# Kernel optimization log

Hardware: AMD Instinct MI355X
Metric: run time of the kernel (lower is better)

Reference implementation:

```python
import jax, jax.numpy as jnp
import numpy as np
from jax import lax

B, L, D = 4, 4096, 1024
EXPAND, K = 2, 4
INNER = D * EXPAND  # 2048


def setup_inputs() -> dict:
    key = jax.random.key(0)
    k0, k1, k2, k3, k4 = jax.random.split(key, 5)
    s = 0.02
    return {
        "x": jax.random.normal(k0, (B, L, D), jnp.float32),
        "W_in": jax.random.normal(k1, (D, 2 * INNER), jnp.float32) * s,
        "conv_w": jax.random.normal(k2, (INNER, 1, K), jnp.float32) * s,  # depthwise [out, in/groups=1, k]
        "conv_b": jax.random.normal(k3, (INNER,), jnp.float32) * s,
        "W_out": jax.random.normal(k4, (INNER, D), jnp.float32) * s,
    }


def reference(x, W_in, conv_w, conv_b, W_out):
    # Linear (no bias): [B,L,D] -> [B,L,2*INNER]
    h = jnp.einsum("bld,df->blf", x, W_in)
    # GLU(dim=-1): first half gated by sigmoid of second half
    a, g = jnp.split(h, 2, axis=-1)
    h = a * jax.nn.sigmoid(g)  # [B,L,INNER]
    # depthwise causal Conv1d: torch pads both sides by K-1 then slices [:, :, :L],
    # which equals left-padding by K-1 only.
    hc = jnp.transpose(h, (0, 2, 1))  # [B,INNER,L]
    y = lax.conv_general_dilated(
        hc, conv_w,
        window_strides=(1,),
        padding=[(K - 1, 0)],
        dimension_numbers=("NCH", "OIH", "NCH"),
        feature_group_count=INNER,
    ) + conv_b[None, :, None]  # [B,INNER,L]
    y = jax.nn.silu(y)
    y = jnp.transpose(y, (0, 2, 1))  # [B,L,INNER]
    # Output linear (no bias): [B,L,INNER] -> [B,L,D]
    return jnp.einsum("blf,fd->bld", y, W_out)
```

## Files before the change

### kernel.cpp

```cpp
#include <hip/hip_runtime.h>
#include <hip/hip_bf16.h>

constexpr int B_ = 4, L_ = 4096, D_ = 1024, INNER_ = 2048;
constexpr int M_ = B_ * L_;
constexpr int N1_ = 2 * INNER_;

typedef __attribute__((ext_vector_type(4))) float f32x4;
typedef __attribute__((ext_vector_type(8))) short short8;

#define DEV static __device__ __forceinline__

DEV short f2bfs(float f) {
  __hip_bfloat16 h = __float2bfloat16(f);
  return __builtin_bit_cast(short, h);
}
DEV float bfs2f(short s) {
  unsigned int u = ((unsigned int)(unsigned short)s) << 16;
  return __builtin_bit_cast(float, u);
}

DEV void gload_lds16(const void* g, void* l) {
  __builtin_amdgcn_global_load_lds(
      (const __attribute__((address_space(1))) unsigned int*)g,
      (__attribute__((address_space(3))) unsigned int*)l,
      16, 0, 0);
}

constexpr int VMW8 = 0x0F78;
constexpr int VMW4 = 0x0F74;
constexpr int VMW0 = 0x0F70;

__global__ void k_cvt(const float4* __restrict__ in, short4* __restrict__ out, int n4) {
  int i = blockIdx.x * blockDim.x + threadIdx.x;
  if (i >= n4) return;
  float4 v = in[i];
  short4 o;
  o.x = f2bfs(v.x); o.y = f2bfs(v.y); o.z = f2bfs(v.z); o.w = f2bfs(v.w);
  out[i] = o;
}

__global__ void k_transpose_cvt(const float* __restrict__ W, short* __restrict__ Wt,
                                int R, int C) {
  __shared__ short tile[32][33];
  int tx = threadIdx.x & 31;
  int ty = threadIdx.x >> 5;
  int c0 = blockIdx.x * 32;
  int r0 = blockIdx.y * 32;
#pragma unroll
  for (int i = 0; i < 32; i += 8)
    tile[ty + i][tx] = f2bfs(W[(size_t)(r0 + ty + i) * C + (c0 + tx)]);
  __syncthreads();
#pragma unroll
  for (int i = 0; i < 32; i += 8)
    Wt[(size_t)(c0 + ty + i) * R + (r0 + tx)] = tile[tx][ty + i];
}

template<int K, bool GLU>
__global__ __launch_bounds__(512, 2) void k_gemm_pipe(
    const short* __restrict__ A, const short* __restrict__ Bt,
    short* __restrict__ OutBf, float* __restrict__ OutF) {
  extern __shared__ char lds[];
  constexpr int NT = K / 32;
  const int tid = threadIdx.x;
  const int wid = tid >> 6, lane = tid & 63;
  const int l16 = lane & 15, kg = lane >> 4;
  const int wr = wid >> 1, wc = wid & 1;

  const int bid = (int)blockIdx.x;
  const int j = bid & 7;
  const int s = bid >> 3;
  const int r = s >> 5;
  const int t = s & 31;
  const int bm = j * 8 + (t >> 2);
  const int bn = r * 4 + (t & 3);
  const int m0 = bm * 256;

  const short* pA[2];
  const short* pB[2];
  int ldsA[2], ldsB[2];
#pragma unroll
  for (int h = 0; h < 2; ++h) {
    int p = h * 512 + wid * 64 + lane;
    int q = p ^ ((p >> 3) & 7);
    int row = q >> 2, c = q & 3;
    pA[h] = A + (size_t)(m0 + row) * K + c * 8;
    int gb;
    if constexpr (GLU) {
      gb = bn * 128 + ((row >> 7) << 6) + (row & 63) + (((row >> 6) & 1) ? 2048 : 0);
    } else {
      gb = bn * 256 + row;
    }
    pB[h] = Bt + (size_t)gb * K + c * 8;
    ldsA[h] = h * 8192 + wid * 1024;
    ldsB[h] = 16384 + h * 8192 + wid * 1024;
  }

  int offA[4], offB[8];
#pragma unroll
  for (int m = 0; m < 4; ++m) {
    int row = wr * 64 + m * 16 + l16;
    int ch = row * 4 + kg;
    offA[m] = (ch ^ ((ch >> 3) & 7)) * 16;
  }
#pragma unroll
  for (int n = 0; n < 8; ++n) {
    int row = wc * 128 + n * 16 + l16;
    int ch = row * 4 + kg;
    offB[n] = 16384 + (ch ^ ((ch >> 3) & 7)) * 16;
  }

  const f32x4 z = {0.f, 0.f, 0.f, 0.f};
  f32x4 acc[4][8];
#pragma unroll
  for (int m = 0; m < 4; ++m)
#pragma unroll
    for (int n = 0; n < 8; ++n) acc[m][n] = z;

#pragma unroll
  for (int tt = 0; tt < 3; ++tt) {
    char* ws = lds + tt * 32768;
#pragma unroll
    for (int h = 0; h < 2; ++h) {
      gload_lds16(pA[h] + tt * 32, ws + ldsA[h]);
      gload_lds16(pB[h] + tt * 32, ws + ldsB[h]);
    }
  }
#pragma unroll
  for (int h = 0; h < 2; ++h) { pA[h] += 96; pB[h] += 96; }

  auto iter = [&](int tt, bool do_stage) {
    __builtin_amdgcn_s_barrier();
    char* slot = lds + (tt & 3) * 32768;
    char* wsl  = lds + ((tt + 3) & 3) * 32768;
    short8 af[4], bfr[4];
#pragma unroll
    for (int m = 0; m < 4; ++m) af[m] = *(const short8*)(slot + offA[m]);
#pragma unroll
    for (int n = 0; n < 4; ++n) bfr[n] = *(const short8*)(slot + offB[n]);
    if (do_stage) {
      gload_lds16(pA[0], wsl + ldsA[0]);
      gload_lds16(pA[1], wsl + ldsA[1]);
    }
    __builtin_amdgcn_s_barrier();
    asm volatile("s_waitcnt lgkmcnt(0)" ::: "memory");
    __builtin_amdgcn_sched_barrier(0);
    __builtin_amdgcn_s_setprio(1);
#pragma unroll
    for (int m = 0; m < 4; ++m)
#pragma unroll
      for (int n = 0; n < 4; ++n)
        acc[m][n] = __builtin_amdgcn_mfma_f32_16x16x32_bf16(af[m], bfr[n], acc[m][n], 0, 0, 0);
    __builtin_amdgcn_s_setprio(0);
    __builtin_amdgcn_s_barrier();
#pragma unroll
    for (int n = 0; n < 4; ++n) bfr[n] = *(const short8*)(slot + offB[4 + n]);
    if (do_stage) {
      gload_lds16(pB[0], wsl + ldsB[0]);
      gload_lds16(pB[1], wsl + ldsB[1]);
      pA[0] += 32; pA[1] += 32; pB[0] += 32; pB[1] += 32;
    }
    __builtin_amdgcn_s_barrier();
    asm volatile("s_waitcnt lgkmcnt(0)" ::: "memory");
    __builtin_amdgcn_sched_barrier(0);
    __builtin_amdgcn_s_setprio(1);
#pragma unroll
    for (int m = 0; m < 4; ++m)
#pragma unroll
      for (int n = 0; n < 4; ++n)
        acc[m][4 + n] = __builtin_amdgcn_mfma_f32_16x16x32_bf16(af[m], bfr[n], acc[m][4 + n], 0, 0, 0);
    __builtin_amdgcn_s_setprio(0);
  };

  for (int tt = 0; tt < NT - 3; ++tt) {
    __builtin_amdgcn_s_waitcnt(VMW8);
    iter(tt, true);
  }
  __builtin_amdgcn_s_waitcnt(VMW8); iter(NT - 3, false);
  __builtin_amdgcn_s_waitcnt(VMW4); iter(NT - 2, false);
  __builtin_amdgcn_s_waitcnt(VMW0); iter(NT - 1, false);

  const int r4 = (lane >> 4) * 4;
  if constexpr (GLU) {
#pragma unroll
    for (int m = 0; m < 4; ++m) {
      const int row = m0 + wr * 64 + m * 16 + r4;
#pragma unroll
      for (int n = 0; n < 4; ++n) {
        const int col = bn * 128 + wc * 64 + n * 16 + l16;
#pragma unroll
        for (int rr = 0; rr < 4; ++rr) {
          float a = acc[m][n][rr];
          float g = acc[m][4 + n][rr];
          OutBf[(size_t)(row + rr) * 2048 + col] = f2bfs(a / (1.f + __expf(-g)));
        }
      }
    }
  } else {
#pragma unroll
    for (int m = 0; m < 4; ++m) {
      const int row = m0 + wr * 64 + m * 16 + r4;
#pragma unroll
      for (int n = 0; n < 8; ++n) {
        const int col = bn * 256 + wc * 128 + n * 16 + l16;
#pragma unroll
        for (int rr = 0; rr < 4; ++rr)
          OutF[(size_t)(row + rr) * 1024 + col] = acc[m][n][rr];
      }
    }
  }
}

__global__ void k_conv_silu(const short* __restrict__ G, const float* __restrict__ w,
                            const float* __restrict__ bias, short* __restrict__ Y) {
  const int t = threadIdx.x;
  const int c0 = t * 8;
  const int b = blockIdx.y;
  const int l0 = blockIdx.x * 16;
  const size_t base = ((size_t)b * L_) * INNER_ + c0;

  float wv[4][8], bv[8];
#pragma unroll
  for (int jj = 0; jj < 8; ++jj) bv[jj] = bias[c0 + jj];
#pragma unroll
  for (int k = 0; k < 4; ++k)
#pragma unroll
    for (int jj = 0; jj < 8; ++jj) wv[k][jj] = w[(c0 + jj) * 4 + k];

  float h[3][8];
#pragma unroll
  for (int p = 0; p < 3; ++p) {
    const int l = l0 - 3 + p;
    if (l < 0) {
#pragma unroll
      for (int jj = 0; jj < 8; ++jj) h[p][jj] = 0.f;
    } else {
      short8 v = *(const short8*)(G + base + (size_t)l * INNER_);
#pragma unroll
      for (int jj = 0; jj < 8; ++jj) h[p][jj] = bfs2f(v[jj]);
    }
  }

  for (int i = 0; i < 16; ++i) {
    const int l = l0 + i;
    short8 v = *(const short8*)(G + base + (size_t)l * INNER_);
    short8 o;
#pragma unroll
    for (int jj = 0; jj < 8; ++jj) {
      float g0 = bfs2f(v[jj]);
      float y = bv[jj] + wv[0][jj] * h[0][jj] + wv[1][jj] * h[1][jj] + wv[2][jj] * h[2][jj] + wv[3][jj] * g0;
      y = y / (1.f + __expf(-y));
      o[jj] = f2bfs(y);
      h[0][jj] = h[1][jj]; h[1][jj] = h[2][jj]; h[2][jj] = g0;
    }
    *(short8*)(Y + base + (size_t)l * INNER_) = o;
  }
}

extern "C" void kernel_launch(void* const* d_in, const int* in_sizes, int n_in,
                              void* d_out, int out_size, void* d_ws, size_t ws_size,
                              hipStream_t stream) {
  (void)in_sizes; (void)n_in; (void)out_size; (void)ws_size;
  const float* x      = (const float*)d_in[0];
  const float* W_in   = (const float*)d_in[1];
  const float* conv_w = (const float*)d_in[2];
  const float* conv_b = (const float*)d_in[3];
  const float* W_out  = (const float*)d_in[4];
  float* out = (float*)d_out;

  char* ws = (char*)d_ws;
  size_t off = 0;
  auto alloc = [&](size_t bytes) {
    char* p = ws + off;
    off += (bytes + 255) & ~(size_t)255;
    return p;
  };
  short* Xb    = (short*)alloc((size_t)M_ * D_ * 2);
  short* WinT  = (short*)alloc((size_t)N1_ * D_ * 2);
  short* WoutT = (short*)alloc((size_t)D_ * INNER_ * 2);
  short* G     = (short*)alloc((size_t)M_ * INNER_ * 2);
  short* Y     = (short*)alloc((size_t)M_ * INNER_ * 2);

  hipFuncSetAttribute((const void*)k_gemm_pipe<1024, true>,
                      hipFuncAttributeMaxDynamicSharedMemorySize, 131072);
  hipFuncSetAttribute((const void*)k_gemm_pipe<2048, false>,
                      hipFuncAttributeMaxDynamicSharedMemorySize, 131072);

  k_cvt<<<(M_ * D_ / 4 + 255) / 256, 256, 0, stream>>>(
      (const float4*)x, (short4*)Xb, M_ * D_ / 4);
  k_transpose_cvt<<<dim3(N1_ / 32, D_ / 32), 256, 0, stream>>>(W_in, WinT, D_, N1_);
  k_transpose_cvt<<<dim3(D_ / 32, INNER_ / 32), 256, 0, stream>>>(W_out, WoutT, INNER_, D_);

  k_gemm_pipe<1024, true><<<1024, 512, 131072, stream>>>(Xb, WinT, G, nullptr);
  k_conv_silu<<<dim3(L_ / 16, B_), 256, 0, stream>>>(G, conv_w, conv_b, Y);
  k_gemm_pipe<2048, false><<<256, 512, 131072, stream>>>(Y, WoutT, nullptr, out);
}
```

Measured before the change: 378.0 us.

## Switch GEMM inner loop to 32x32x16 MFMA and drop mid-iteration barriers

Replaces the 16x16x32 bf16 MFMA tiling with 32x32x16 MFMA, so each wave issues fewer, larger matrix instructions per 64x128 tile and needs fewer LDS fragment reads per FLOP. The two-phase iteration with its extra s_barriers and sched_barriers is collapsed into a single phase. All global->LDS staging for a slot is now issued up front, and two K-halves are read before one MFMA burst. The epilogue row/column mapping is rewritten for the 32x32 accumulator layout. Removing the intermediate barriers risks weaker overlap control or LDS hazards. The larger fragments hold more registers live at once.

```diff
diff --git a/kernel.cpp b/kernel.cpp
--- a/kernel.cpp
+++ b/kernel.cpp
@@ -6,6 +6,7 @@
 constexpr int N1_ = 2 * INNER_;
 
 typedef __attribute__((ext_vector_type(4))) float f32x4;
+typedef __attribute__((ext_vector_type(16))) float f32x16;
 typedef __attribute__((ext_vector_type(8))) short short8;
 
 #define DEV static __device__ __forceinline__
@@ -63,7 +64,7 @@
   constexpr int NT = K / 32;
   const int tid = threadIdx.x;
   const int wid = tid >> 6, lane = tid & 63;
-  const int l16 = lane & 15, kg = lane >> 4;
+  const int l32 = lane & 31, kh = lane >> 5;
   const int wr = wid >> 1, wc = wid & 1;
 
   const int bid = (int)blockIdx.x;
@@ -95,26 +96,31 @@
     ldsB[h] = 16384 + h * 8192 + wid * 1024;
   }
 
-  int offA[4], offB[8];
-#pragma unroll
-  for (int m = 0; m < 4; ++m) {
-    int row = wr * 64 + m * 16 + l16;
-    int ch = row * 4 + kg;
-    offA[m] = (ch ^ ((ch >> 3) & 7)) * 16;
-  }
-#pragma unroll
-  for (int n = 0; n < 8; ++n) {
-    int row = wc * 128 + n * 16 + l16;
-    int ch = row * 4 + kg;
-    offB[n] = 16384 + (ch ^ ((ch >> 3) & 7)) * 16;
-  }
-
-  const f32x4 z = {0.f, 0.f, 0.f, 0.f};
-  f32x4 acc[4][8];
-#pragma unroll
-  for (int m = 0; m < 4; ++m)
-#pragma unroll
-    for (int n = 0; n < 8; ++n) acc[m][n] = z;
+  int offA[2][2], offB[4][2];
+#pragma unroll
+  for (int m = 0; m < 2; ++m)
+#pragma unroll
+    for (int ks = 0; ks < 2; ++ks) {
+      int row = wr * 64 + m * 32 + l32;
+      int ch = row * 4 + ks * 2 + kh;
+      offA[m][ks] = (ch ^ ((ch >> 3) & 7)) * 16;
+    }
+#pragma unroll
+  for (int n = 0; n < 4; ++n)
+#pragma unroll
+    for (int ks = 0; ks < 2; ++ks) {
+      int row = wc * 128 + n * 32 + l32;
+      int ch = row * 4 + ks * 2 + kh;
+      offB[n][ks] = 16384 + (ch ^ ((ch >> 3) & 7)) * 16;
+    }
+
+  f32x16 acc[2][4];
+#pragma unroll
+  for (int m = 0; m < 2; ++m)
+#pragma unroll
+    for (int n = 0; n < 4; ++n)
+#pragma unroll
+      for (int e = 0; e < 16; ++e) acc[m][n][e] = 0.f;
 
 #pragma unroll
   for (int tt = 0; tt < 3; ++tt) {
@@ -132,43 +138,35 @@
     __builtin_amdgcn_s_barrier();
     char* slot = lds + (tt & 3) * 32768;
     char* wsl  = lds + ((tt + 3) & 3) * 32768;
-    short8 af[4], bfr[4];
-#pragma unroll
-    for (int m = 0; m < 4; ++m) af[m] = *(const short8*)(slot + offA[m]);
-#pragma unroll
-    for (int n = 0; n < 4; ++n) bfr[n] = *(const short8*)(slot + offB[n]);
+    short8 a0[2], a1[2], b0[4], b1[4];
+#pragma unroll
+    for (int m = 0; m < 2; ++m) a0[m] = *(const short8*)(slot + offA[m][0]);
+#pragma unroll
+    for (int n = 0; n < 4; ++n) b0[n] = *(const short8*)(slot + offB[n][0]);
     if (do_stage) {
       gload_lds16(pA[0], wsl + ldsA[0]);
       gload_lds16(pA[1], wsl + ldsA[1]);
-    }
-    __builtin_amdgcn_s_barrier();
-    asm volatile("s_waitcnt lgkmcnt(0)" ::: "memory");
-    __builtin_amdgcn_sched_barrier(0);
-    __builtin_amdgcn_s_setprio(1);
-#pragma unroll
-    for (int m = 0; m < 4; ++m)
-#pragma unroll
-      for (int n = 0; n < 4; ++n)
-        acc[m][n] = __builtin_amdgcn_mfma_f32_16x16x32_bf16(af[m], bfr[n], acc[m][n], 0, 0, 0);
-    __builtin_amdgcn_s_setprio(0);
-    __builtin_amdgcn_s_barrier();
-#pragma unroll
-    for (int n = 0; n < 4; ++n) bfr[n] = *(const short8*)(slot + offB[4 + n]);
-    if (do_stage) {
       gload_lds16(pB[0], wsl + ldsB[0]);
       gload_lds16(pB[1], wsl + ldsB[1]);
       pA[0] += 32; pA[1] += 32; pB[0] += 32; pB[1] += 32;
     }
-    __builtin_amdgcn_s_barrier();
+#pragma unroll
+    for (int m = 0; m < 2; ++m) a1[m] = *(const short8*)(slot + offA[m][1]);
+#pragma unroll
+    for (int n = 0; n < 4; ++n) b1[n] = *(const short8*)(slot + offB[n][1]);
+    __builtin_amdgcn_s_setprio(1);
+#pragma unroll
+    for (int m = 0; m < 2; ++m)
+#pragma unroll
+      for (int n = 0; n < 4; ++n)
+        acc[m][n] = __builtin_amdgcn_mfma_f32_32x32x16_bf16(a0[m], b0[n], acc[m][n], 0, 0, 0);
+#pragma unroll
+    for (int m = 0; m < 2; ++m)
+#pragma unroll
+      for (int n = 0; n < 4; ++n)
+        acc[m][n] = __builtin_amdgcn_mfma_f32_32x32x16_bf16(a1[m], b1[n], acc[m][n], 0, 0, 0);
+    __builtin_amdgcn_s_setprio(0);
     asm volatile("s_waitcnt lgkmcnt(0)" ::: "memory");
-    __builtin_amdgcn_sched_barrier(0);
-    __builtin_amdgcn_s_setprio(1);
-#pragma unroll
-    for (int m = 0; m < 4; ++m)
-#pragma unroll
-      for (int n = 0; n < 4; ++n)
-        acc[m][4 + n] = __builtin_amdgcn_mfma_f32_16x16x32_bf16(af[m], bfr[n], acc[m][4 + n], 0, 0, 0);
-    __builtin_amdgcn_s_setprio(0);
   };
 
   for (int tt = 0; tt < NT - 3; ++tt) {
@@ -179,34 +177,32 @@
   __builtin_amdgcn_s_waitcnt(VMW4); iter(NT - 2, false);
   __builtin_amdgcn_s_waitcnt(VMW0); iter(NT - 1, false);
 
-  const int r4 = (lane >> 4) * 4;
   if constexpr (GLU) {
 #pragma unroll
-    for (int m = 0; m < 4; ++m) {
-      const int row = m0 + wr * 64 + m * 16 + r4;
-#pragma unroll
-      for (int n = 0; n < 4; ++n) {
-        const int col = bn * 128 + wc * 64 + n * 16 + l16;
-#pragma unroll
-        for (int rr = 0; rr < 4; ++rr) {
-          float a = acc[m][n][rr];
-          float g = acc[m][4 + n][rr];
-          OutBf[(size_t)(row + rr) * 2048 + col] = f2bfs(a / (1.f + __expf(-g)));
+    for (int m = 0; m < 2; ++m)
+#pragma unroll
+      for (int n = 0; n < 2; ++n) {
+        const f32x16 Aa = acc[m][n];
+        const f32x16 Gg = acc[m][n + 2];
+        const int col = bn * 128 + wc * 64 + n * 32 + l32;
+#pragma unroll
+        for (int reg = 0; reg < 16; ++reg) {
+          const int row = m0 + wr * 64 + m * 32 + (reg & 3) + ((reg >> 2) << 3) + (kh << 2);
+          OutBf[(size_t)row * 2048 + col] = f2bfs(Aa[reg] / (1.f + __expf(-Gg[reg])));
         }
       }
-    }
   } else {
 #pragma unroll
-    for (int m = 0; m < 4; ++m) {
-      const int row = m0 + wr * 64 + m * 16 + r4;
-#pragma unroll
-      for (int n = 0; n < 8; ++n) {
-        const int col = bn * 256 + wc * 128 + n * 16 + l16;
-#pragma unroll
-        for (int rr = 0; rr < 4; ++rr)
-          OutF[(size_t)(row + rr) * 1024 + col] = acc[m][n][rr];
+    for (int m = 0; m < 2; ++m)
+#pragma unroll
+      for (int n = 0; n < 4; ++n) {
+        const int col = bn * 256 + wc * 128 + n * 32 + l32;
+#pragma unroll
+        for (int reg = 0; reg < 16; ++reg) {
+          const int row = m0 + wr * 64 + m * 32 + (reg & 3) + ((reg >> 2) << 3) + (kh << 2);
+          OutF[(size_t)row * 1024 + col] = acc[m][n][reg];
+        }
       }
-    }
   }
 }
 
```

After: 376.7 us. About the same (-0.3%).
